# Optimization experiments

Measured on AMD Instinct MI355X. Metric: run time of the kernel, lower is better.

## Reference

```python
import jax, jax.numpy as jnp
import numpy as np

D_MODEL = 1024
NUM_HEADS = 16
D_K = D_MODEL // NUM_HEADS  # 64


def setup_inputs() -> dict:
    key = jax.random.key(0)
    ks = jax.random.split(key, 12)
    B, S = 4, 2048
    scale = 1.0 / np.sqrt(D_MODEL)
    inp = {
        'query': jax.random.normal(ks[0], (B, S, D_MODEL), jnp.float32),
        'key': jax.random.normal(ks[1], (B, S, D_MODEL), jnp.float32),
        'value': jax.random.normal(ks[2], (B, S, D_MODEL), jnp.float32),
        # per-head projection weights stacked along head axis [H, d_model, d_k]
        'Wq': jax.random.normal(ks[3], (NUM_HEADS, D_MODEL, D_K), jnp.float32) * scale,
        'bq': jax.random.normal(ks[4], (NUM_HEADS, D_K), jnp.float32) * 0.01,
        'Wk': jax.random.normal(ks[5], (NUM_HEADS, D_MODEL, D_K), jnp.float32) * scale,
        'bk': jax.random.normal(ks[6], (NUM_HEADS, D_K), jnp.float32) * 0.01,
        'Wv': jax.random.normal(ks[7], (NUM_HEADS, D_MODEL, D_K), jnp.float32) * scale,
        'bv': jax.random.normal(ks[8], (NUM_HEADS, D_K), jnp.float32) * 0.01,
        'Wo': jax.random.normal(ks[9], (NUM_HEADS * D_K, D_MODEL), jnp.float32) * scale,
        'bo': jax.random.normal(ks[10], (D_MODEL,), jnp.float32) * 0.01,
    }
    return inp


def reference(query, key, value, Wq, bq, Wk, bk, Wv, bv, Wo, bo):
    # Per-head linear projections, batched over heads: [B,S,D] x [H,D,K] -> [B,H,S,K]
    q = jnp.einsum('bsd,hdk->bhsk', query, Wq) + bq[None, :, None, :]
    k = jnp.einsum('bsd,hdk->bhsk', key, Wk) + bk[None, :, None, :]
    v = jnp.einsum('bsd,hdk->bhsk', value, Wv) + bv[None, :, None, :]
    # Scaled dot-product attention per head
    scores = jnp.einsum('bhqk,bhsk->bhqs', q, k) / jnp.sqrt(jnp.asarray(D_K, q.dtype))
    attn = jax.nn.softmax(scores, axis=-1)
    heads = jnp.einsum('bhqs,bhsk->bhqk', attn, v)  # [B,H,S,K]
    # Concat heads -> [B,S,H*K], then output projection
    B, H, S, K = heads.shape
    concat = jnp.transpose(heads, (0, 2, 1, 3)).reshape(B, S, H * K)
    return concat @ Wo + bo
```

## Files before the change

kernel.cpp:

```cpp
#include <hip/hip_runtime.h>
#include <hip/hip_bf16.h>

typedef __bf16 bf16_t;
typedef __bf16 bf16x8 __attribute__((ext_vector_type(8)));
typedef __bf16 bf16x4 __attribute__((ext_vector_type(4)));
typedef float f32x4 __attribute__((ext_vector_type(4)));
typedef float f32x16 __attribute__((ext_vector_type(16)));

constexpr int BB = 4;
constexpr int SS = 2048;
constexpr int DM = 1024;
constexpr int NH = 16;
constexpr int DK = 64;
constexpr int MROWS = BB * SS;

template <int N> struct IC { static constexpr int V = N; };

__device__ inline uint32_t pkbf16(float a, float b) {
    union { bf16_t h[2]; uint32_t u; } x;
    x.h[0] = (bf16_t)a; x.h[1] = (bf16_t)b;
    return x.u;
}

__device__ inline void gld16(const bf16_t* g, bf16_t* l) {
    __builtin_amdgcn_global_load_lds((const __attribute__((address_space(1))) void*)g,
                                     (__attribute__((address_space(3))) void*)l, 16, 0, 0);
}

__device__ inline f32x16 mfma32(bf16x8 a, bf16x8 b, f32x16 c) {
    return __builtin_amdgcn_mfma_f32_32x32x16_bf16(a, b, c, 0, 0, 0);
}

__device__ inline bf16x8 lds_rd(const bf16_t* base, int row, int slot) {
    return *(const bf16x8*)((const char*)base + row * 128 + ((slot ^ (row & 7)) << 4));
}

__global__ __launch_bounds__(256) void k_transpose3(const float* __restrict__ s0,
                                                    const float* __restrict__ s1,
                                                    const float* __restrict__ s2,
                                                    bf16_t* __restrict__ dst) {
    __shared__ float tile[32][33];
    const int zz = blockIdx.z;
    const int zt = zz >> 4, zh = zz & 15;
    const float* src = (zt == 0) ? s0 : ((zt == 1) ? s1 : s2);
    const int cb = blockIdx.x * 32, rb = blockIdx.y * 32;
    const long zoff = (long)zh * DM * DK;
    bf16_t* d = dst + (size_t)zt * DM * DM + (size_t)zh * DK * DM;
    const int tx = threadIdx.x & 31, ty = threadIdx.x >> 5;
#pragma unroll
    for (int i = 0; i < 4; ++i) {
        int r = rb + ty + i * 8;
        tile[ty + i * 8][tx] = src[zoff + (long)r * DK + cb + tx];
    }
    __syncthreads();
#pragma unroll
    for (int i = 0; i < 4; ++i) {
        int c = cb + ty + i * 8;
        d[(long)c * DM + rb + tx] = (bf16_t)tile[tx][ty + i * 8];
    }
}

__global__ __launch_bounds__(256) void k_transpose(const float* __restrict__ src,
                                                   bf16_t* __restrict__ dst,
                                                   int R, int C) {
    __shared__ float tile[32][33];
    const int cb = blockIdx.x * 32, rb = blockIdx.y * 32;
    const int tx = threadIdx.x & 31, ty = threadIdx.x >> 5;
#pragma unroll
    for (int i = 0; i < 4; ++i) {
        int r = rb + ty + i * 8;
        tile[ty + i * 8][tx] = src[(long)r * C + cb + tx];
    }
    __syncthreads();
#pragma unroll
    for (int i = 0; i < 4; ++i) {
        int c = cb + ty + i * 8;
        dst[(long)c * R + rb + tx] = (bf16_t)tile[tx][ty + i * 8];
    }
}

__global__ __launch_bounds__(256) void k_proj(
    const float* __restrict__ Aq, const float* __restrict__ Ak, const float* __restrict__ Av,
    const bf16_t* __restrict__ Wt,
    const float* __restrict__ bq, const float* __restrict__ bk, const float* __restrict__ bv,
    bf16_t* __restrict__ qkv) {
    const int hwid = blockIdx.x;
    const int c = hwid & 7, j = hwid >> 3;
    const int z = j >> 6;
    const int r = j & 63;
    const int n0 = (r & 7) * 128;
    const int m0 = (c * 8 + (r >> 3)) * 128;

    const float* A = (z == 0) ? Aq : ((z == 1) ? Ak : Av);
    const float* bias = (z == 0) ? bq : ((z == 1) ? bk : bv);
    const float scale = (z == 0) ? (float)(1.4426950408889634 / 8.0) : 1.0f;
    const bf16_t* Bt = Wt + (size_t)z * DM * DM;
    bf16_t* outp = qkv + (size_t)z * BB * NH * SS * DK;

    __shared__ __align__(16) union SM {
        struct { bf16_t a[128][72]; bf16_t b[128][64]; } s;
        bf16_t vt[128][136];
    } sm;

    const int t = threadIdx.x;
    const int lane = t & 63, w = t >> 6;
    const int lr = lane & 15, lg = lane >> 4;
    const int wr = w >> 1, wc = w & 1;

    f32x4 acc[4][4] = {};

    for (int kt = 0; kt < 16; ++kt) {
        const int k0 = kt * 64;
#pragma unroll
        for (int p = 0; p < 4; ++p) {
            int id = p * 256 + t;
            int row = id >> 3, ssl = id & 7;
            gld16(&Bt[(size_t)(n0 + row) * DM + k0 + ((ssl ^ (row & 7)) << 3)],
                  &sm.s.b[0][0] + (size_t)(p * 256 + w * 64) * 8);
        }
#pragma unroll
        for (int p = 0; p < 8; ++p) {
            int idx = p * 256 + t;
            int rr = idx >> 4, seg = idx & 15;
            const float4 v = *(const float4*)&A[(size_t)(m0 + rr) * DM + k0 + seg * 4];
            bf16x4 pk = {(bf16_t)v.x, (bf16_t)v.y, (bf16_t)v.z, (bf16_t)v.w};
            *(bf16x4*)&sm.s.a[rr][seg * 4] = pk;
        }
        __syncthreads();
#pragma unroll
        for (int ks = 0; ks < 2; ++ks) {
            const int lk = ks * 32 + lg * 8;
            bf16x8 af[4], bfm[4];
#pragma unroll
            for (int i = 0; i < 4; ++i) af[i] = *(const bf16x8*)&sm.s.a[wr * 64 + i * 16 + lr][lk];
#pragma unroll
            for (int jj = 0; jj < 4; ++jj) bfm[jj] = lds_rd(&sm.s.b[0][0], wc * 64 + jj * 16 + lr, ks * 4 + lg);
#pragma unroll
            for (int i = 0; i < 4; ++i)
#pragma unroll
                for (int jj = 0; jj < 4; ++jj)
                    acc[i][jj] = __builtin_amdgcn_mfma_f32_16x16x32_bf16(af[i], bfm[jj], acc[i][jj], 0, 0, 0);
        }
        __syncthreads();
    }
    const int b = m0 >> 11, s0 = m0 & (SS - 1);
    if (z == 2) {
#pragma unroll
        for (int i = 0; i < 4; ++i)
#pragma unroll
            for (int jj = 0; jj < 4; ++jj) {
                int col = wc * 64 + jj * 16 + lr;
                float bv_ = bias[n0 + col];
#pragma unroll
                for (int rr = 0; rr < 4; ++rr)
                    sm.vt[col][wr * 64 + i * 16 + lg * 4 + rr] = (bf16_t)(acc[i][jj][rr] + bv_);
            }
        __syncthreads();
#pragma unroll
        for (int pp = 0; pp < 8; ++pp) {
            int d = pp * 16 + (t >> 4);
            int cs = (t & 15) * 8;
            bf16x8 v = *(const bf16x8*)&sm.vt[d][cs];
            int h = (n0 + d) >> 6, dd = d & 63;
            *(bf16x8*)&outp[((size_t)(b * NH + h) * DK + dd) * SS + s0 + cs] = v;
        }
    } else {
#pragma unroll
        for (int i = 0; i < 4; ++i) {
#pragma unroll
            for (int jj = 0; jj < 4; ++jj) {
                int col = wc * 64 + jj * 16 + lr;
                int h = (n0 + col) >> 6, ko = col & 63;
                float bv_ = bias[n0 + col];
#pragma unroll
                for (int rr = 0; rr < 4; ++rr) {
                    int s = s0 + wr * 64 + i * 16 + lg * 4 + rr;
                    float v = (acc[i][jj][rr] + bv_) * scale;
                    outp[(((size_t)b * NH + h) * SS + s) * DK + ko] = (bf16_t)v;
                }
            }
        }
    }
}

__global__ __launch_bounds__(256, 4) void k_attn(const bf16_t* __restrict__ qkv,
                                                 bf16_t* __restrict__ concat) {
    const int hw = blockIdx.x + 16 * (blockIdx.y + 16 * blockIdx.z);
    const int lb = (hw & 7) * 128 + (hw >> 3);
    const int qt = lb & 15;
    const int h = (lb >> 4) & 15;
    const int b = lb >> 8;

    const size_t PH = (size_t)BB * NH * SS * DK;
    const bf16_t* qp = qkv + ((size_t)(b * NH + h) * SS) * DK;
    const bf16_t* kp = qp + PH;
    const bf16_t* vtp = qkv + 2 * PH + (size_t)(b * NH + h) * DK * SS;

    __shared__ __align__(16) bf16_t k_lds[2][4096];
    __shared__ __align__(16) bf16_t v_lds[2][4096];

    const int t = threadIdx.x;
    const int lane = t & 63, w = t >> 6;
    const int l31 = lane & 31;
    const bool hf = (lane >> 5) != 0;

    const int sr = t >> 3, ssl = t & 7;
    const int prow = (sr & ~12) | ((sr & 4) << 1) | ((sr & 8) >> 1);
    const int ssw = (ssl ^ (sr & 7)) * 8;
    const size_t okA = (size_t)prow * DK + ssw;
    const size_t ovA = (size_t)sr * SS + ssw;

    const int qbase = qt * 128 + w * 32;
    bf16x8 qf[4];
#pragma unroll
    for (int ks = 0; ks < 4; ++ks)
        qf[ks] = *(const bf16x8*)&qp[(size_t)(qbase + l31) * DK + ks * 16 + (hf ? 8 : 0)];

    f32x16 oacc0 = {}, oacc1 = {};
    f32x16 lacc = {};

    bf16x8 vone;
#pragma unroll
    for (int i = 0; i < 8; ++i) vone[i] = (l31 == 0) ? (bf16_t)1.0f : (bf16_t)0.0f;

    constexpr int NT = SS / 64;

    gld16(kp + okA, &k_lds[0][w * 512]);
    gld16(kp + okA + 32 * DK, &k_lds[0][w * 512 + 2048]);
    gld16(vtp + ovA, &v_lds[0][w * 512]);
    gld16(vtp + ovA + (size_t)32 * SS, &v_lds[0][w * 512 + 2048]);
    __syncthreads();

    auto body = [&](auto icur, int it) {
        constexpr int cur = decltype(icur)::V;
        if (it + 1 < NT) {
            const bf16_t* kt_ = kp + (size_t)(it + 1) * 4096;
            const bf16_t* vt_ = vtp + (size_t)(it + 1) * 64;
            gld16(kt_ + okA, &k_lds[cur ^ 1][w * 512]);
            gld16(kt_ + okA + 32 * DK, &k_lds[cur ^ 1][w * 512 + 2048]);
            gld16(vt_ + ovA, &v_lds[cur ^ 1][w * 512]);
            gld16(vt_ + ovA + (size_t)32 * SS, &v_lds[cur ^ 1][w * 512 + 2048]);
        }
        f32x16 sc0 = {}, sc1 = {};
        __builtin_amdgcn_s_setprio(1);
#pragma unroll
        for (int ks = 0; ks < 4; ++ks) {
            bf16x8 kf0 = lds_rd(k_lds[cur], l31, 2 * ks + hf);
            bf16x8 kf1 = lds_rd(k_lds[cur], 32 + l31, 2 * ks + hf);
            sc0 = mfma32(kf0, qf[ks], sc0);
            sc1 = mfma32(kf1, qf[ks], sc1);
        }
        __builtin_amdgcn_s_setprio(0);
        uint32_t wk[16];
#pragma unroll
        for (int pr = 0; pr < 8; ++pr)
            wk[pr] = pkbf16(exp2f(sc0[2 * pr]), exp2f(sc0[2 * pr + 1]));
#pragma unroll
        for (int pr = 0; pr < 8; ++pr)
            wk[8 + pr] = pkbf16(exp2f(sc1[2 * pr]), exp2f(sc1[2 * pr + 1]));
        __builtin_amdgcn_s_setprio(1);
#pragma unroll
        for (int kq = 0; kq < 4; ++kq) {
            union { uint32_t u[4]; bf16x8 v; } pb;
#pragma unroll
            for (int i = 0; i < 4; ++i) pb.u[i] = wk[kq * 4 + i];
            bf16x8 vf0 = lds_rd(v_lds[cur], l31, 2 * kq + hf);
            bf16x8 vf1 = lds_rd(v_lds[cur], 32 + l31, 2 * kq + hf);
            oacc0 = mfma32(vf0, pb.v, oacc0);
            oacc1 = mfma32(vf1, pb.v, oacc1);
            lacc = mfma32(vone, pb.v, lacc);
        }
        __builtin_amdgcn_s_setprio(0);
        __syncthreads();
    };

#pragma unroll 1
    for (int t2 = 0; t2 < NT; t2 += 2) {
        body(IC<0>{}, t2);
        body(IC<1>{}, t2 + 1);
    }

    float l = __shfl(lacc[0], l31);
    float inv = 1.0f / l;
    const int q = qbase + l31;
#pragma unroll
    for (int dt = 0; dt < 2; ++dt) {
#pragma unroll
        for (int quad = 0; quad < 4; ++quad) {
            const f32x16& oa = dt ? oacc1 : oacc0;
            bf16x4 ov = {(bf16_t)(oa[quad * 4 + 0] * inv),
                         (bf16_t)(oa[quad * 4 + 1] * inv),
                         (bf16_t)(oa[quad * 4 + 2] * inv),
                         (bf16_t)(oa[quad * 4 + 3] * inv)};
            int col = dt * 32 + quad * 8 + (hf ? 4 : 0);
            *(bf16x4*)&concat[((size_t)b * SS + q) * DM + h * 64 + col] = ov;
        }
    }
}

__global__ __launch_bounds__(256) void k_out(const bf16_t* __restrict__ Ab,
                                             const bf16_t* __restrict__ Wot,
                                             const float* __restrict__ bo,
                                             float* __restrict__ out) {
    const int hwid = blockIdx.x;
    const int c = hwid & 7, j = hwid >> 3;
    const int n0 = (j & 7) * 128;
    const int m0 = (c * 8 + (j >> 3)) * 128;

    __shared__ __align__(16) bf16_t a_lds[128 * 64];
    __shared__ __align__(16) bf16_t b_lds[128 * 64];

    const int t = threadIdx.x;
    const int lane = t & 63, w = t >> 6;
    const int lr = lane & 15, lg = lane >> 4;
    const int wr = w >> 1, wc = w & 1;

    f32x4 acc[4][4] = {};

    for (int kt = 0; kt < 16; ++kt) {
        const int k0 = kt * 64;
#pragma unroll
        for (int p = 0; p < 4; ++p) {
            int id = p * 256 + t;
            int row = id >> 3, ssl = id & 7;
            int sc = (ssl ^ (row & 7)) << 3;
            gld16(&Ab[(size_t)(m0 + row) * DM + k0 + sc], a_lds + (size_t)(p * 256 + w * 64) * 8);
            gld16(&Wot[(size_t)(n0 + row) * DM + k0 + sc], b_lds + (size_t)(p * 256 + w * 64) * 8);
        }
        __syncthreads();
#pragma unroll
        for (int ks = 0; ks < 2; ++ks) {
            bf16x8 af[4], bfm[4];
#pragma unroll
            for (int i = 0; i < 4; ++i) af[i] = lds_rd(a_lds, wr * 64 + i * 16 + lr, ks * 4 + lg);
#pragma unroll
            for (int jj = 0; jj < 4; ++jj) bfm[jj] = lds_rd(b_lds, wc * 64 + jj * 16 + lr, ks * 4 + lg);
#pragma unroll
            for (int i = 0; i < 4; ++i)
#pragma unroll
                for (int jj = 0; jj < 4; ++jj)
                    acc[i][jj] = __builtin_amdgcn_mfma_f32_16x16x32_bf16(af[i], bfm[jj], acc[i][jj], 0, 0, 0);
        }
        __syncthreads();
    }
#pragma unroll
    for (int i = 0; i < 4; ++i) {
#pragma unroll
        for (int jj = 0; jj < 4; ++jj) {
            int col = n0 + wc * 64 + jj * 16 + lr;
            float bv_ = bo[col];
#pragma unroll
            for (int rr = 0; rr < 4; ++rr) {
                int mrow = m0 + wr * 64 + i * 16 + lg * 4 + rr;
                out[(size_t)mrow * DM + col] = acc[i][jj][rr] + bv_;
            }
        }
    }
}

extern "C" void kernel_launch(void* const* d_in, const int* in_sizes, int n_in,
                              void* d_out, int out_size, void* d_ws, size_t ws_size,
                              hipStream_t stream) {
    const float* query = (const float*)d_in[0];
    const float* key   = (const float*)d_in[1];
    const float* value = (const float*)d_in[2];
    const float* Wq = (const float*)d_in[3];
    const float* bq = (const float*)d_in[4];
    const float* Wk = (const float*)d_in[5];
    const float* bk = (const float*)d_in[6];
    const float* Wv = (const float*)d_in[7];
    const float* bv = (const float*)d_in[8];
    const float* Wo = (const float*)d_in[9];
    const float* bo = (const float*)d_in[10];

    char* ws = (char*)d_ws;
    bf16_t* qkv    = (bf16_t*)ws;
    bf16_t* Wt     = (bf16_t*)(ws + (size_t)50331648);
    bf16_t* Wot    = (bf16_t*)(ws + (size_t)50331648 + 6291456);
    bf16_t* concat = (bf16_t*)(ws + (size_t)50331648 + 8388608);

    k_transpose3<<<dim3(2, 32, 48), 256, 0, stream>>>(Wq, Wk, Wv, Wt);
    k_transpose<<<dim3(32, 32, 1), 256, 0, stream>>>(Wo, Wot, DM, DM);

    k_proj<<<dim3(1536), 256, 0, stream>>>(query, key, value, Wt, bq, bk, bv, qkv);
    k_attn<<<dim3(16, 16, 4), 256, 0, stream>>>(qkv, concat);
    k_out<<<dim3(512), 256, 0, stream>>>(concat, Wot, bo, (float*)d_out);
}
```

Baseline: 223.3 us.

## Double-buffer weight tiles and register-prefetch activations in QKV projection GEMM

Restructures the QKV projection main loop so the next K-tile of the bf16 weight is loaded asynchronously into a second LDS buffer, and the next fp32 activation tile is held in registers, while MFMAs run on the current tile. The activations are converted and written to LDS after the compute finishes. The goal is to hide global-load latency behind compute. In exchange it uses more LDS and registers and adds an extra barrier per iteration.

```diff
diff --git a/kernel.cpp b/kernel.cpp
--- a/kernel.cpp
+++ b/kernel.cpp
@@ -98,7 +98,7 @@
     bf16_t* outp = qkv + (size_t)z * BB * NH * SS * DK;
 
     __shared__ __align__(16) union SM {
-        struct { bf16_t a[128][72]; bf16_t b[128][64]; } s;
+        struct { bf16_t a[128][72]; bf16_t b[2][8192]; } s;
         bf16_t vt[128][136];
     } sm;
 
@@ -108,25 +108,36 @@
     const int wr = w >> 1, wc = w & 1;
 
     f32x4 acc[4][4] = {};
-
-    for (int kt = 0; kt < 16; ++kt) {
-        const int k0 = kt * 64;
-#pragma unroll
-        for (int p = 0; p < 4; ++p) {
-            int id = p * 256 + t;
-            int row = id >> 3, ssl = id & 7;
-            gld16(&Bt[(size_t)(n0 + row) * DM + k0 + ((ssl ^ (row & 7)) << 3)],
-                  &sm.s.b[0][0] + (size_t)(p * 256 + w * 64) * 8);
-        }
-#pragma unroll
-        for (int p = 0; p < 8; ++p) {
-            int idx = p * 256 + t;
-            int rr = idx >> 4, seg = idx & 15;
-            const float4 v = *(const float4*)&A[(size_t)(m0 + rr) * DM + k0 + seg * 4];
-            bf16x4 pk = {(bf16_t)v.x, (bf16_t)v.y, (bf16_t)v.z, (bf16_t)v.w};
-            *(bf16x4*)&sm.s.a[rr][seg * 4] = pk;
-        }
-        __syncthreads();
+    float4 apf[8];
+
+    const int brow = t >> 3, bssl = t & 7;
+    const size_t bsrc = (size_t)(n0 + brow) * DM + ((bssl ^ (brow & 7)) << 3);
+    const int ar0 = t >> 4, aseg = t & 15;
+
+#pragma unroll
+    for (int p = 0; p < 4; ++p)
+        gld16(&Bt[bsrc + p * 32 * DM], &sm.s.b[0][(p * 256 + w * 64) * 8]);
+#pragma unroll
+    for (int p = 0; p < 8; ++p)
+        apf[p] = *(const float4*)&A[(size_t)(m0 + ar0 + p * 16) * DM + aseg * 4];
+#pragma unroll
+    for (int p = 0; p < 8; ++p) {
+        bf16x4 pk = {(bf16_t)apf[p].x, (bf16_t)apf[p].y, (bf16_t)apf[p].z, (bf16_t)apf[p].w};
+        *(bf16x4*)&sm.s.a[ar0 + p * 16][aseg * 4] = pk;
+    }
+    __syncthreads();
+
+    auto body = [&](auto icur, int kt) {
+        constexpr int cur = decltype(icur)::V;
+        const int k1 = (kt + 1) * 64;
+        if (kt + 1 < 16) {
+#pragma unroll
+            for (int p = 0; p < 4; ++p)
+                gld16(&Bt[bsrc + k1 + p * 32 * DM], &sm.s.b[cur ^ 1][(p * 256 + w * 64) * 8]);
+#pragma unroll
+            for (int p = 0; p < 8; ++p)
+                apf[p] = *(const float4*)&A[(size_t)(m0 + ar0 + p * 16) * DM + k1 + aseg * 4];
+        }
 #pragma unroll
         for (int ks = 0; ks < 2; ++ks) {
             const int lk = ks * 32 + lg * 8;
@@ -134,7 +145,7 @@
 #pragma unroll
             for (int i = 0; i < 4; ++i) af[i] = *(const bf16x8*)&sm.s.a[wr * 64 + i * 16 + lr][lk];
 #pragma unroll
-            for (int jj = 0; jj < 4; ++jj) bfm[jj] = lds_rd(&sm.s.b[0][0], wc * 64 + jj * 16 + lr, ks * 4 + lg);
+            for (int jj = 0; jj < 4; ++jj) bfm[jj] = lds_rd(sm.s.b[cur], wc * 64 + jj * 16 + lr, ks * 4 + lg);
 #pragma unroll
             for (int i = 0; i < 4; ++i)
 #pragma unroll
@@ -142,7 +153,22 @@
                     acc[i][jj] = __builtin_amdgcn_mfma_f32_16x16x32_bf16(af[i], bfm[jj], acc[i][jj], 0, 0, 0);
         }
         __syncthreads();
-    }
+        if (kt + 1 < 16) {
+#pragma unroll
+            for (int p = 0; p < 8; ++p) {
+                bf16x4 pk = {(bf16_t)apf[p].x, (bf16_t)apf[p].y, (bf16_t)apf[p].z, (bf16_t)apf[p].w};
+                *(bf16x4*)&sm.s.a[ar0 + p * 16][aseg * 4] = pk;
+            }
+        }
+        __syncthreads();
+    };
+
+#pragma unroll 1
+    for (int kt = 0; kt < 16; kt += 2) {
+        body(IC<0>{}, kt);
+        body(IC<1>{}, kt + 1);
+    }
+
     const int b = m0 >> 11, s0 = m0 & (SS - 1);
     if (z == 2) {
 #pragma unroll
```

Result: faster. 214.4 us (-4.0%).
